# Performance work log

Measured on AMD Instinct MI355X. Metric: run time of the kernel, lower is better.

The kernel has to match this reference:

```python
import jax, jax.numpy as jnp
import numpy as np

N_NODES = 100000
N_EDGES = 1000000
NUM_FEATURES = 64
HIDDEN = 64
NUM_GRAPHS = 128


def setup_inputs() -> dict:
    key = jax.random.key(0)
    ks = jax.random.split(key, 12)
    x = jax.random.normal(ks[0], (N_NODES, NUM_FEATURES), dtype=jnp.float32)
    edge_index = jax.random.randint(ks[1], (2, N_EDGES), 0, N_NODES, dtype=jnp.int64)
    edge_weight = jax.random.uniform(ks[2], (N_EDGES,), dtype=jnp.float32)
    batch = jnp.sort(jax.random.randint(ks[3], (N_NODES,), 0, NUM_GRAPHS, dtype=jnp.int64))
    s1 = 1.0 / np.sqrt(NUM_FEATURES)
    s2 = 1.0 / np.sqrt(HIDDEN)
    # GraphConv layer 1: lin_rel (with bias) applied to aggregated msgs, lin_root (no bias)
    w1_rel = jax.random.uniform(ks[4], (HIDDEN, NUM_FEATURES), jnp.float32, -s1, s1)
    b1_rel = jax.random.uniform(ks[5], (HIDDEN,), jnp.float32, -s1, s1)
    w1_root = jax.random.uniform(ks[6], (HIDDEN, NUM_FEATURES), jnp.float32, -s1, s1)
    # GraphConv layer 2
    w2_rel = jax.random.uniform(ks[7], (HIDDEN, HIDDEN), jnp.float32, -s2, s2)
    b2_rel = jax.random.uniform(ks[8], (HIDDEN,), jnp.float32, -s2, s2)
    w2_root = jax.random.uniform(ks[9], (HIDDEN, HIDDEN), jnp.float32, -s2, s2)
    # final Linear(hidden, 1)
    w_lin = jax.random.uniform(ks[10], (1, HIDDEN), jnp.float32, -s2, s2)
    b_lin = jax.random.uniform(ks[11], (1,), jnp.float32, -s2, s2)
    return {
        "x": x, "edge_index": edge_index, "edge_weight": edge_weight, "batch": batch,
        "w1_rel": w1_rel, "b1_rel": b1_rel, "w1_root": w1_root,
        "w2_rel": w2_rel, "b2_rel": b2_rel, "w2_root": w2_root,
        "w_lin": w_lin, "b_lin": b_lin,
    }


def graph_conv(x, edge_index, edge_weight, w_rel, b_rel, w_root):
    # messages: x[src] * e, scatter-add into dst  (gather-scale-scatter)
    src, dst = edge_index[0], edge_index[1]
    msgs = x[src] * edge_weight[:, None]                      # [E, F]
    aggr = jax.ops.segment_sum(msgs, dst, num_segments=x.shape[0])  # [N, F]
    return aggr @ w_rel.T + b_rel + x @ w_root.T


def reference(x, edge_index, edge_weight, batch,
              w1_rel, b1_rel, w1_root, w2_rel, b2_rel, w2_root, w_lin, b_lin):
    h = graph_conv(x, edge_index, edge_weight, w1_rel, b1_rel, w1_root)
    h = jax.nn.relu(h)
    h = graph_conv(h, edge_index, edge_weight, w2_rel, b2_rel, w2_root)
    # global_mean_pool over graph ids
    sums = jax.ops.segment_sum(h, batch, num_segments=NUM_GRAPHS)          # [G, H]
    counts = jax.ops.segment_sum(jnp.ones((h.shape[0],), h.dtype), batch,
                                 num_segments=NUM_GRAPHS)                  # [G]
    pooled = sums / jnp.maximum(counts, 1.0)[:, None]
    # dropout(p=0.5) in eval mode is identity
    return pooled @ w_lin.T + b_lin                                        # [G, 1]
```

## Files before the change

### kernel.cpp

```cpp
#include <hip/hip_runtime.h>
#include <hip/hip_bf16.h>


#define N_NODES 100000
#define N_EDGES 1000000
#define NGRAPHS 128
#define BN 512
#define NBUCK ((N_NODES + BN - 1) / BN)
#define FILL_T 16
#define FILL_TILE (256 * FILL_T)
#define FILL_NB ((N_EDGES + FILL_TILE - 1) / FILL_TILE)
#define NTILES (N_NODES / 16)
#define AST 72

typedef __attribute__((ext_vector_type(8))) short bf16x8;
typedef __attribute__((ext_vector_type(8))) unsigned short u16x8;
typedef __attribute__((ext_vector_type(4))) float f32x4;

__device__ __forceinline__ unsigned short f2bf(float f) {
    unsigned u = __float_as_uint(f);
    unsigned r = (u + 0x7FFFu + ((u >> 16) & 1u)) >> 16;
    return (unsigned short)r;
}
__device__ __forceinline__ float bf2f(unsigned short h) {
    return __uint_as_float(((unsigned)h) << 16);
}

__global__ __launch_bounds__(256) void prep_cvt_kernel(
    const float* __restrict__ x, unsigned short* __restrict__ xh, int n8,
    const float* __restrict__ w1rel, const float* __restrict__ w1root,
    const float* __restrict__ w2rel, const float* __restrict__ w2root,
    const float* __restrict__ wlin, const float* __restrict__ b2rel,
    const float* __restrict__ blin, unsigned short* __restrict__ whirel,
    unsigned short* __restrict__ wlorel, unsigned short* __restrict__ whiroot,
    unsigned short* __restrict__ wloroot, float* __restrict__ u,
    float* __restrict__ v, float* __restrict__ C) {
    int tid = threadIdx.x;
    int i = blockIdx.x * 256 + tid;
    if (i < n8) {
        const float4* xp = (const float4*)x + (size_t)i * 2;
        float4 a = xp[0], b = xp[1];
        u16x8 o;
        o[0] = f2bf(a.x); o[1] = f2bf(a.y); o[2] = f2bf(a.z); o[3] = f2bf(a.w);
        o[4] = f2bf(b.x); o[5] = f2bf(b.y); o[6] = f2bf(b.z); o[7] = f2bf(b.w);
        *((u16x8*)xh + i) = o;
        return;
    }
    for (int k = tid; k < 4096; k += 256) {
        float a = w1rel[k];
        unsigned short hi = f2bf(a);
        whirel[k] = hi;
        wlorel[k] = f2bf(a - bf2f(hi));
        float b = w1root[k];
        unsigned short hb = f2bf(b);
        whiroot[k] = hb;
        wloroot[k] = f2bf(b - bf2f(hb));
    }
    if (tid < 64) {
        float uu = 0.f, vv = 0.f;
        for (int h = 0; h < 64; ++h) {
            float wl = wlin[h];
            uu += wl * w2rel[h * 64 + tid];
            vv += wl * w2root[h * 64 + tid];
        }
        u[tid] = uu;
        v[tid] = vv;
    }
    if (tid == 0) {
        float c = blin[0];
        for (int h = 0; h < 64; ++h) c += wlin[h] * b2rel[h];
        *C = c;
    }
}

__global__ __launch_bounds__(256) void bucket_hist(const int* __restrict__ ei,
                                                   int* __restrict__ bcount,
                                                   int E) {
    __shared__ int lh[NBUCK];
    int tid = threadIdx.x;
    for (int i = tid; i < NBUCK; i += 256) lh[i] = 0;
    __syncthreads();
    for (int e = blockIdx.x * 256 + tid; e < E; e += gridDim.x * 256)
        atomicAdd(&lh[ei[E + e] >> 9], 1);
    __syncthreads();
    for (int i = tid; i < NBUCK; i += 256) {
        int c = lh[i];
        if (c) atomicAdd(&bcount[i], c);
    }
}

__global__ void bucket_scan(const int* __restrict__ bcount,
                            int* __restrict__ boff, int* __restrict__ cursor) {
    __shared__ int s[256];
    int t = threadIdx.x;
    int v = (t < NBUCK) ? bcount[t] : 0;
    s[t] = v;
    __syncthreads();
    for (int off = 1; off < 256; off <<= 1) {
        int x = (t >= off) ? s[t - off] : 0;
        __syncthreads();
        s[t] += x;
        __syncthreads();
    }
    if (t < NBUCK) {
        boff[t] = s[t] - v;
        cursor[t] = s[t] - v;
    }
    if (t == 255) boff[NBUCK] = s[255];
}

__global__ __launch_bounds__(256) void bucket_fill(
    const int* __restrict__ ei, const float* __restrict__ ew,
    int* __restrict__ cursor, int2* __restrict__ ebuf, int E) {
    __shared__ int lh[NBUCK];
    __shared__ int gbase[NBUCK];
    int tid = threadIdx.x;
    for (int i = tid; i < NBUCK; i += 256) lh[i] = 0;
    __syncthreads();
    int base = blockIdx.x * FILL_TILE;
    int2 rec[FILL_T];
    int meta[FILL_T];
#pragma unroll
    for (int i = 0; i < FILL_T; ++i) {
        int e = base + i * 256 + tid;
        meta[i] = -1;
        if (e < E) {
            int src = ei[e];
            int dst = ei[E + e];
            int b = dst >> 9;
            int r = atomicAdd(&lh[b], 1);
            rec[i].x = src | ((dst & (BN - 1)) << 17);
            rec[i].y = __float_as_int(ew[e]);
            meta[i] = (b << 13) | r;
        }
    }
    __syncthreads();
    for (int i = tid; i < NBUCK; i += 256) {
        int c = lh[i];
        gbase[i] = c ? atomicAdd(&cursor[i], c) : 0;
    }
    __syncthreads();
#pragma unroll
    for (int i = 0; i < FILL_T; ++i) {
        if (meta[i] >= 0) {
            int b = meta[i] >> 13;
            int r = meta[i] & 8191;
            ebuf[gbase[b] + r] = rec[i];
        }
    }
}

__global__ __launch_bounds__(512) void csr_build(
    const int* __restrict__ boff, const int2* __restrict__ ebuf,
    const int* __restrict__ batch, int* __restrict__ row_ptr,
    int2* __restrict__ csr, int N) {
    __shared__ int s[BN];
    int b = blockIdx.x;
    int t = threadIdx.x;
    int beg = boff[b], end = boff[b + 1];
    s[t] = 0;
    __syncthreads();
    for (int j = beg + t; j < end; j += 512)
        atomicAdd(&s[(ebuf[j].x >> 17) & (BN - 1)], 1);
    __syncthreads();
    int v = s[t];
    for (int off = 1; off < BN; off <<= 1) {
        int x = (t >= off) ? s[t - off] : 0;
        __syncthreads();
        s[t] += x;
        __syncthreads();
    }
    int excl = s[t] - v;
    int gidx = b * BN + t;
    if (gidx <= N) row_ptr[gidx] = beg + excl;
    __syncthreads();
    s[t] = excl;
    __syncthreads();
    for (int j = beg + t; j < end; j += 512) {
        int2 rec = ebuf[j];
        int dlo = (rec.x >> 17) & (BN - 1);
        int g = batch[b * BN + dlo];
        int r = atomicAdd(&s[dlo], 1);
        int2 o;
        o.x = (rec.x & 0x1FFFF) | (g << 17);
        o.y = rec.y;
        csr[beg + r] = o;
    }
}

__global__ __launch_bounds__(256) void gather_dense_kernel(
    const unsigned short* __restrict__ xh, const int* __restrict__ row_ptr,
    const int2* __restrict__ csr, const unsigned short* __restrict__ whirel,
    const unsigned short* __restrict__ wlorel,
    const unsigned short* __restrict__ whiroot,
    const unsigned short* __restrict__ wloroot,
    const float* __restrict__ b1rel, const float* __restrict__ u,
    const float* __restrict__ v, float* __restrict__ p, float* __restrict__ q,
    int ntiles) {
    __shared__ unsigned short arow[4][16 * AST];
    int lane = threadIdx.x & 63;
    int wv = threadIdx.x >> 6;
    int wave = (blockIdx.x << 2) + wv;
    if (wave >= ntiles) return;
    unsigned short* my = &arow[wv][0];
    int nb = wave * 16;
    int g = lane >> 4;
    int c = lane & 15;

    for (int nl = 0; nl < 16; ++nl) {
        int node = nb + nl;
        int beg = row_ptr[node], end = row_ptr[node + 1];
        float4 acc = {0.f, 0.f, 0.f, 0.f};
        for (int j0 = beg; j0 < end; j0 += 64) {
            int cnt = min(64, end - j0);
            int2 e = {0, 0};
            if (lane < cnt) e = csr[j0 + lane];
            for (int k = 0; k < cnt; k += 4) {
                int myk = k + g;
                int sj = __shfl(e.x, myk) & 0x1FFFF;
                float wj = __int_as_float(__shfl(e.y, myk));
                if (myk < cnt) {
                    ushort4 xv =
                        *(const ushort4*)(xh + (size_t)sj * 64 + c * 4);
                    acc.x += wj * bf2f(xv.x);
                    acc.y += wj * bf2f(xv.y);
                    acc.z += wj * bf2f(xv.z);
                    acc.w += wj * bf2f(xv.w);
                }
            }
        }
#pragma unroll
        for (int off = 16; off < 64; off <<= 1) {
            acc.x += __shfl_xor(acc.x, off);
            acc.y += __shfl_xor(acc.y, off);
            acc.z += __shfl_xor(acc.z, off);
            acc.w += __shfl_xor(acc.w, off);
        }
        if (lane < 16) {
            ushort4 o;
            o.x = f2bf(acc.x);
            o.y = f2bf(acc.y);
            o.z = f2bf(acc.z);
            o.w = f2bf(acc.w);
            *(ushort4*)(my + nl * AST + c * 4) = o;
        }
    }

    int lo4 = lane & 15;
    int quad = lane >> 4;
    f32x4 acc4[4];
#pragma unroll
    for (int t = 0; t < 4; ++t) acc4[t] = (f32x4){0.f, 0.f, 0.f, 0.f};
#pragma unroll
    for (int s = 0; s < 2; ++s) {
        bf16x8 Aa = *(const bf16x8*)(my + lo4 * AST + s * 32 + quad * 8);
        bf16x8 Ax = *(const bf16x8*)(xh + (size_t)(nb + lo4) * 64 + s * 32 +
                                     quad * 8);
#pragma unroll
        for (int t = 0; t < 4; ++t) {
            int off = (t * 16 + lo4) * 64 + s * 32 + quad * 8;
            bf16x8 bhr = *(const bf16x8*)(whirel + off);
            bf16x8 blr = *(const bf16x8*)(wlorel + off);
            bf16x8 bhx = *(const bf16x8*)(whiroot + off);
            bf16x8 blx = *(const bf16x8*)(wloroot + off);
            acc4[t] = __builtin_amdgcn_mfma_f32_16x16x32_bf16(Aa, bhr, acc4[t],
                                                              0, 0, 0);
            acc4[t] = __builtin_amdgcn_mfma_f32_16x16x32_bf16(Aa, blr, acc4[t],
                                                              0, 0, 0);
            acc4[t] = __builtin_amdgcn_mfma_f32_16x16x32_bf16(Ax, bhx, acc4[t],
                                                              0, 0, 0);
            acc4[t] = __builtin_amdgcn_mfma_f32_16x16x32_bf16(Ax, blx, acc4[t],
                                                              0, 0, 0);
        }
    }

    float pc[4] = {0.f, 0.f, 0.f, 0.f};
    float qc[4] = {0.f, 0.f, 0.f, 0.f};
#pragma unroll
    for (int t = 0; t < 4; ++t) {
        float bb = b1rel[t * 16 + lo4];
        float uu = u[t * 16 + lo4];
        float vv = v[t * 16 + lo4];
#pragma unroll
        for (int r = 0; r < 4; ++r) {
            float h1 = fmaxf(acc4[t][r] + bb, 0.f);
            pc[r] += uu * h1;
            qc[r] += vv * h1;
        }
    }
#pragma unroll
    for (int off = 1; off < 16; off <<= 1) {
#pragma unroll
        for (int r = 0; r < 4; ++r) {
            pc[r] += __shfl_xor(pc[r], off);
            qc[r] += __shfl_xor(qc[r], off);
        }
    }
    if (lo4 == 0) {
        f32x4 po = {pc[0], pc[1], pc[2], pc[3]};
        f32x4 qo = {qc[0], qc[1], qc[2], qc[3]};
        *(f32x4*)(p + nb + quad * 4) = po;
        *(f32x4*)(q + nb + quad * 4) = qo;
    }
}

#define PT_EPT 4
#define PT_EPW (64 * PT_EPT)
#define PT_NB ((N_EDGES + 4 * PT_EPW - 1) / (4 * PT_EPW))
#define PS_NB 98
__global__ __launch_bounds__(256) void pool_both(
    const int2* __restrict__ csr, const float* __restrict__ p,
    const float* __restrict__ q, const int* __restrict__ batch,
    float* __restrict__ gp, float* __restrict__ gq, float* __restrict__ gc,
    int E, int N) {
    __shared__ float lbuf[2 * NGRAPHS];
    int tid = threadIdx.x;
    lbuf[tid] = 0.f;
    __syncthreads();
    if (blockIdx.x < PT_NB) {
        int lane = tid & 63;
        int wid = (blockIdx.x * 256 + tid) >> 6;
        int base = wid * PT_EPW;
        float acc = 0.f;
        int curg = -1;
#pragma unroll
        for (int i = 0; i < PT_EPT; ++i) {
            int j = base + i * 64 + lane;
            if (j < E) {
                int2 e = csr[j];
                int g = ((unsigned)e.x) >> 17;
                float val = __int_as_float(e.y) * p[e.x & 0x1FFFF];
                if (g != curg) {
                    if (curg >= 0) atomicAdd(&lbuf[curg], acc);
                    curg = g;
                    acc = 0.f;
                }
                acc += val;
            }
        }
        if (curg >= 0) atomicAdd(&lbuf[curg], acc);
        __syncthreads();
        if (tid < NGRAPHS) {
            float t = lbuf[tid];
            if (t != 0.f) atomicAdd(&gp[tid], t);
        }
    } else {
        int bid = blockIdx.x - PT_NB;
        for (int i = bid * 256 + tid; i < N; i += PS_NB * 256) {
            int g = batch[i];
            atomicAdd(&lbuf[g], q[i]);
            atomicAdd(&lbuf[NGRAPHS + g], 1.f);
        }
        __syncthreads();
        if (tid < NGRAPHS) {
            if (lbuf[NGRAPHS + tid] != 0.f) {
                atomicAdd(&gq[tid], lbuf[tid]);
                atomicAdd(&gc[tid], lbuf[NGRAPHS + tid]);
            }
        }
    }
}

__global__ void final_kernel(const float* __restrict__ gp,
                             const float* __restrict__ gq,
                             const float* __restrict__ gc,
                             const float* __restrict__ C,
                             float* __restrict__ out) {
    int g = threadIdx.x;
    float c = fmaxf(gc[g], 1.0f);
    out[g] = (gp[g] + gq[g]) / c + *C;
}

extern "C" void kernel_launch(void* const* d_in, const int* in_sizes, int n_in,
                              void* d_out, int out_size, void* d_ws,
                              size_t ws_size, hipStream_t stream) {
    const float* x      = (const float*)d_in[0];
    const int*   ei     = (const int*)d_in[1];
    const float* ew     = (const float*)d_in[2];
    const int*   batch  = (const int*)d_in[3];
    const float* w1rel  = (const float*)d_in[4];
    const float* b1rel  = (const float*)d_in[5];
    const float* w1root = (const float*)d_in[6];
    const float* w2rel  = (const float*)d_in[7];
    const float* b2rel  = (const float*)d_in[8];
    const float* w2root = (const float*)d_in[9];
    const float* wlin   = (const float*)d_in[10];
    const float* blin   = (const float*)d_in[11];
    float* out = (float*)d_out;

    char* wsb = (char*)d_ws;
    int2* csr  = (int2*)wsb;
    int2* ebuf = (int2*)(wsb + (size_t)N_EDGES * 8);
    char* tail = wsb + (size_t)N_EDGES * 16;
    unsigned short* whirel  = (unsigned short*)tail;
    unsigned short* wlorel  = whirel + 4096;
    unsigned short* whiroot = wlorel + 4096;
    unsigned short* wloroot = whiroot + 4096;
    float* p  = (float*)(wloroot + 4096);
    float* q  = p + N_NODES;
    float* u  = q + N_NODES;
    float* v  = u + 64;
    float* C  = v + 64;
    int*   bcount = (int*)(C + 1);
    float* gp = (float*)(bcount + NBUCK);
    float* gq = gp + NGRAPHS;
    float* gc = gq + NGRAPHS;
    int*   boff   = (int*)(gc + NGRAPHS);
    int*   cursor = boff + (NBUCK + 1);
    int*   row_ptr = cursor + NBUCK;
    unsigned short* xh = (unsigned short*)(row_ptr + N_NODES + 2);

    hipMemsetAsync(bcount, 0, (NBUCK + 3 * NGRAPHS) * sizeof(int), stream);

    int n8 = N_NODES * 64 / 8;
    prep_cvt_kernel<<<n8 / 256 + 1, 256, 0, stream>>>(
        x, xh, n8, w1rel, w1root, w2rel, w2root, wlin, b2rel, blin, whirel,
        wlorel, whiroot, wloroot, u, v, C);

    bucket_hist<<<256, 256, 0, stream>>>(ei, bcount, N_EDGES);
    bucket_scan<<<1, 256, 0, stream>>>(bcount, boff, cursor);
    bucket_fill<<<FILL_NB, 256, 0, stream>>>(ei, ew, cursor, ebuf, N_EDGES);
    csr_build<<<NBUCK, 512, 0, stream>>>(boff, ebuf, batch, row_ptr, csr,
                                         N_NODES);

    gather_dense_kernel<<<(NTILES + 3) / 4, 256, 0, stream>>>(
        xh, row_ptr, csr, whirel, wlorel, whiroot, wloroot, b1rel, u, v, p, q,
        NTILES);

    pool_both<<<PT_NB + PS_NB, 256, 0, stream>>>(csr, p, q, batch, gp, gq, gc,
                                                 N_EDGES, N_NODES);
    final_kernel<<<1, NGRAPHS, 0, stream>>>(gp, gq, gc, C, out);
}
```

Baseline: 223.1 us.

## Gather whole 16-node tile edges at once with LDS float atomics

The gather kernel no longer walks the 16 nodes of a tile one at a time with a per-node edge loop and a cross-lane reduction. It now streams all edges of the tile in 64-edge chunks and scatters weighted features into a per-wave fp32 LDS accumulator using shared-memory atomics. To support this, the CSR fill step packs each edge's local destination row into bits 24-27, and the pool kernel masks the graph id accordingly. This removes the divergence and underused lanes caused by short per-node loops, but it adds LDS atomic contention, a larger fp32 LDS footprint, and a float-to-bf16 conversion when building the MFMA A operand.

```diff
diff --git a/kernel.cpp b/kernel.cpp
--- a/kernel.cpp
+++ b/kernel.cpp
@@ -11,7 +11,7 @@
 #define FILL_TILE (256 * FILL_T)
 #define FILL_NB ((N_EDGES + FILL_TILE - 1) / FILL_TILE)
 #define NTILES (N_NODES / 16)
-#define AST 72
+#define AST 68
 
 typedef __attribute__((ext_vector_type(8))) short bf16x8;
 typedef __attribute__((ext_vector_type(8))) unsigned short u16x8;
@@ -182,7 +182,7 @@
         int g = batch[b * BN + dlo];
         int r = atomicAdd(&s[dlo], 1);
         int2 o;
-        o.x = (rec.x & 0x1FFFF) | (g << 17);
+        o.x = (rec.x & 0x1FFFF) | (g << 17) | ((dlo & 15) << 24);
         o.y = rec.y;
         csr[beg + r] = o;
     }
@@ -197,52 +197,38 @@
     const float* __restrict__ b1rel, const float* __restrict__ u,
     const float* __restrict__ v, float* __restrict__ p, float* __restrict__ q,
     int ntiles) {
-    __shared__ unsigned short arow[4][16 * AST];
+    __shared__ float accs[4][16 * AST];
     int lane = threadIdx.x & 63;
     int wv = threadIdx.x >> 6;
     int wave = (blockIdx.x << 2) + wv;
     if (wave >= ntiles) return;
-    unsigned short* my = &arow[wv][0];
+    float* my = &accs[wv][0];
     int nb = wave * 16;
     int g = lane >> 4;
     int c = lane & 15;
 
-    for (int nl = 0; nl < 16; ++nl) {
-        int node = nb + nl;
-        int beg = row_ptr[node], end = row_ptr[node + 1];
-        float4 acc = {0.f, 0.f, 0.f, 0.f};
-        for (int j0 = beg; j0 < end; j0 += 64) {
-            int cnt = min(64, end - j0);
-            int2 e = {0, 0};
-            if (lane < cnt) e = csr[j0 + lane];
-            for (int k = 0; k < cnt; k += 4) {
-                int myk = k + g;
-                int sj = __shfl(e.x, myk) & 0x1FFFF;
-                float wj = __int_as_float(__shfl(e.y, myk));
-                if (myk < cnt) {
-                    ushort4 xv =
-                        *(const ushort4*)(xh + (size_t)sj * 64 + c * 4);
-                    acc.x += wj * bf2f(xv.x);
-                    acc.y += wj * bf2f(xv.y);
-                    acc.z += wj * bf2f(xv.z);
-                    acc.w += wj * bf2f(xv.w);
-                }
+    for (int i = lane; i < 16 * AST; i += 64) my[i] = 0.f;
+
+    int ebeg = row_ptr[nb], eend = row_ptr[nb + 16];
+    for (int j0 = ebeg; j0 < eend; j0 += 64) {
+        int cnt = min(64, eend - j0);
+        int2 e = {0, 0};
+        if (lane < cnt) e = csr[j0 + lane];
+#pragma unroll
+        for (int r = 0; r < 16; ++r) {
+            int myk = r * 4 + g;
+            int ex = __shfl(e.x, myk);
+            float wj = __int_as_float(__shfl(e.y, myk));
+            if (myk < cnt) {
+                int sj = ex & 0x1FFFF;
+                int dl = (ex >> 24) & 15;
+                ushort4 xv = *(const ushort4*)(xh + (size_t)sj * 64 + c * 4);
+                float* dst = my + dl * AST + c * 4;
+                atomicAdd(dst + 0, wj * bf2f(xv.x));
+                atomicAdd(dst + 1, wj * bf2f(xv.y));
+                atomicAdd(dst + 2, wj * bf2f(xv.z));
+                atomicAdd(dst + 3, wj * bf2f(xv.w));
             }
-        }
-#pragma unroll
-        for (int off = 16; off < 64; off <<= 1) {
-            acc.x += __shfl_xor(acc.x, off);
-            acc.y += __shfl_xor(acc.y, off);
-            acc.z += __shfl_xor(acc.z, off);
-            acc.w += __shfl_xor(acc.w, off);
-        }
-        if (lane < 16) {
-            ushort4 o;
-            o.x = f2bf(acc.x);
-            o.y = f2bf(acc.y);
-            o.z = f2bf(acc.z);
-            o.w = f2bf(acc.w);
-            *(ushort4*)(my + nl * AST + c * 4) = o;
         }
     }
 
@@ -253,7 +239,10 @@
     for (int t = 0; t < 4; ++t) acc4[t] = (f32x4){0.f, 0.f, 0.f, 0.f};
 #pragma unroll
     for (int s = 0; s < 2; ++s) {
-        bf16x8 Aa = *(const bf16x8*)(my + lo4 * AST + s * 32 + quad * 8);
+        const float* ap = my + lo4 * AST + s * 32 + quad * 8;
+        bf16x8 Aa;
+#pragma unroll
+        for (int j = 0; j < 8; ++j) Aa[j] = (short)f2bf(ap[j]);
         bf16x8 Ax = *(const bf16x8*)(xh + (size_t)(nb + lo4) * 64 + s * 32 +
                                      quad * 8);
 #pragma unroll
@@ -328,7 +317,7 @@
             int j = base + i * 64 + lane;
             if (j < E) {
                 int2 e = csr[j];
-                int g = ((unsigned)e.x) >> 17;
+                int g = (e.x >> 17) & 127;
                 float val = __int_as_float(e.y) * p[e.x & 0x1FFFF];
                 if (g != curg) {
                     if (curg >= 0) atomicAdd(&lbuf[curg], acc);
```

After: 546.4 us. 2.45x slower.

## Split fused gather+MFMA kernel into separate gather and dense kernels

Applied to the files above, without the earlier changes.

The fused gather/dense kernel is split in two. A gather kernel writes bf16 aggregated features to a global buffer, using a fixed 2048-block grid where each wave handles a contiguous chunk of nodes. A separate MFMA dense kernel then reads that buffer. The aggregation buffer reuses the ebuf workspace region, and the graph id is masked in the pool kernel. The aim is better load balance and occupancy for the gather, at the cost of an extra global round trip (about 12.8 MB) and one more launch.

```diff
diff --git a/kernel.cpp b/kernel.cpp
--- a/kernel.cpp
+++ b/kernel.cpp
@@ -10,8 +10,6 @@
 #define FILL_T 16
 #define FILL_TILE (256 * FILL_T)
 #define FILL_NB ((N_EDGES + FILL_TILE - 1) / FILL_TILE)
-#define NTILES (N_NODES / 16)
-#define AST 72
 
 typedef __attribute__((ext_vector_type(8))) short bf16x8;
 typedef __attribute__((ext_vector_type(8))) unsigned short u16x8;
@@ -188,27 +186,17 @@
     }
 }
 
-__global__ __launch_bounds__(256) void gather_dense_kernel(
+__global__ __launch_bounds__(256) void gather_kernel(
     const unsigned short* __restrict__ xh, const int* __restrict__ row_ptr,
-    const int2* __restrict__ csr, const unsigned short* __restrict__ whirel,
-    const unsigned short* __restrict__ wlorel,
-    const unsigned short* __restrict__ whiroot,
-    const unsigned short* __restrict__ wloroot,
-    const float* __restrict__ b1rel, const float* __restrict__ u,
-    const float* __restrict__ v, float* __restrict__ p, float* __restrict__ q,
-    int ntiles) {
-    __shared__ unsigned short arow[4][16 * AST];
+    const int2* __restrict__ csr, unsigned short* __restrict__ aggr, int N,
+    int chunk) {
     int lane = threadIdx.x & 63;
-    int wv = threadIdx.x >> 6;
-    int wave = (blockIdx.x << 2) + wv;
-    if (wave >= ntiles) return;
-    unsigned short* my = &arow[wv][0];
-    int nb = wave * 16;
+    int wid = (blockIdx.x * blockDim.x + threadIdx.x) >> 6;
     int g = lane >> 4;
     int c = lane & 15;
-
-    for (int nl = 0; nl < 16; ++nl) {
-        int node = nb + nl;
+    int n0 = wid * chunk;
+    int n1 = min(n0 + chunk, N);
+    for (int node = n0; node < n1; ++node) {
         int beg = row_ptr[node], end = row_ptr[node + 1];
         float4 acc = {0.f, 0.f, 0.f, 0.f};
         for (int j0 = beg; j0 < end; j0 += 64) {
@@ -242,18 +230,35 @@
             o.y = f2bf(acc.y);
             o.z = f2bf(acc.z);
             o.w = f2bf(acc.w);
-            *(ushort4*)(my + nl * AST + c * 4) = o;
-        }
-    }
-
+            *(ushort4*)(aggr + (size_t)node * 64 + c * 4) = o;
+        }
+    }
+}
+
+__global__ __launch_bounds__(256, 2) void dense_kernel(
+    const unsigned short* __restrict__ aggr,
+    const unsigned short* __restrict__ xh,
+    const unsigned short* __restrict__ whirel,
+    const unsigned short* __restrict__ wlorel,
+    const unsigned short* __restrict__ whiroot,
+    const unsigned short* __restrict__ wloroot,
+    const float* __restrict__ b1rel, const float* __restrict__ u,
+    const float* __restrict__ v, float* __restrict__ p, float* __restrict__ q,
+    int N) {
+    int lane = threadIdx.x & 63;
+    int wave = (blockIdx.x << 2) + (threadIdx.x >> 6);
+    int nb = wave * 16;
+    if (nb >= N) return;
     int lo4 = lane & 15;
     int quad = lane >> 4;
-    f32x4 acc4[4];
-#pragma unroll
-    for (int t = 0; t < 4; ++t) acc4[t] = (f32x4){0.f, 0.f, 0.f, 0.f};
-#pragma unroll
+
+    f32x4 acc[4];
+#pragma unroll
+    for (int t = 0; t < 4; ++t) acc[t] = (f32x4){0.f, 0.f, 0.f, 0.f};
+
     for (int s = 0; s < 2; ++s) {
-        bf16x8 Aa = *(const bf16x8*)(my + lo4 * AST + s * 32 + quad * 8);
+        bf16x8 Aa = *(const bf16x8*)(aggr + (size_t)(nb + lo4) * 64 + s * 32 +
+                                     quad * 8);
         bf16x8 Ax = *(const bf16x8*)(xh + (size_t)(nb + lo4) * 64 + s * 32 +
                                      quad * 8);
 #pragma unroll
@@ -263,14 +268,14 @@
             bf16x8 blr = *(const bf16x8*)(wlorel + off);
             bf16x8 bhx = *(const bf16x8*)(whiroot + off);
             bf16x8 blx = *(const bf16x8*)(wloroot + off);
-            acc4[t] = __builtin_amdgcn_mfma_f32_16x16x32_bf16(Aa, bhr, acc4[t],
-                                                              0, 0, 0);
-            acc4[t] = __builtin_amdgcn_mfma_f32_16x16x32_bf16(Aa, blr, acc4[t],
-                                                              0, 0, 0);
-            acc4[t] = __builtin_amdgcn_mfma_f32_16x16x32_bf16(Ax, bhx, acc4[t],
-                                                              0, 0, 0);
-            acc4[t] = __builtin_amdgcn_mfma_f32_16x16x32_bf16(Ax, blx, acc4[t],
-                                                              0, 0, 0);
+            acc[t] = __builtin_amdgcn_mfma_f32_16x16x32_bf16(Aa, bhr, acc[t],
+                                                             0, 0, 0);
+            acc[t] = __builtin_amdgcn_mfma_f32_16x16x32_bf16(Aa, blr, acc[t],
+                                                             0, 0, 0);
+            acc[t] = __builtin_amdgcn_mfma_f32_16x16x32_bf16(Ax, bhx, acc[t],
+                                                             0, 0, 0);
+            acc[t] = __builtin_amdgcn_mfma_f32_16x16x32_bf16(Ax, blx, acc[t],
+                                                             0, 0, 0);
         }
     }
 
@@ -283,7 +288,7 @@
         float vv = v[t * 16 + lo4];
 #pragma unroll
         for (int r = 0; r < 4; ++r) {
-            float h1 = fmaxf(acc4[t][r] + bb, 0.f);
+            float h1 = fmaxf(acc[t][r] + bb, 0.f);
             pc[r] += uu * h1;
             qc[r] += vv * h1;
         }
@@ -328,7 +333,7 @@
             int j = base + i * 64 + lane;
             if (j < E) {
                 int2 e = csr[j];
-                int g = ((unsigned)e.x) >> 17;
+                int g = (e.x >> 17) & 127;
                 float val = __int_as_float(e.y) * p[e.x & 0x1FFFF];
                 if (g != curg) {
                     if (curg >= 0) atomicAdd(&lbuf[curg], acc);
@@ -390,8 +395,9 @@
 
     char* wsb = (char*)d_ws;
     int2* csr  = (int2*)wsb;
-    int2* ebuf = (int2*)(wsb + (size_t)N_EDGES * 8);
-    char* tail = wsb + (size_t)N_EDGES * 16;
+    unsigned short* aggr = (unsigned short*)(wsb + (size_t)N_EDGES * 8);
+    int2* ebuf = (int2*)aggr;
+    char* tail = wsb + (size_t)N_EDGES * 8 + (size_t)N_NODES * 128;
     unsigned short* whirel  = (unsigned short*)tail;
     unsigned short* wlorel  = whirel + 4096;
     unsigned short* whiroot = wlorel + 4096;
@@ -423,10 +429,20 @@
     csr_build<<<NBUCK, 512, 0, stream>>>(boff, ebuf, batch, row_ptr, csr,
                                          N_NODES);
 
-    gather_dense_kernel<<<(NTILES + 3) / 4, 256, 0, stream>>>(
-        xh, row_ptr, csr, whirel, wlorel, whiroot, wloroot, b1rel, u, v, p, q,
-        NTILES);
-
+    {
+        int blocks = 2048;
+        int waves = blocks * 4;
+        int chunk = (N_NODES + waves - 1) / waves;
+        gather_kernel<<<blocks, 256, 0, stream>>>(xh, row_ptr, csr, aggr,
+                                                  N_NODES, chunk);
+    }
+    {
+        int tiles = N_NODES / 16;
+        int blocks = (tiles + 3) / 4;
+        dense_kernel<<<blocks, 256, 0, stream>>>(aggr, xh, whirel, wlorel,
+                                                 whiroot, wloroot, b1rel, u, v,
+                                                 p, q, N_NODES);
+    }
     pool_both<<<PT_NB + PS_NB, 256, 0, stream>>>(csr, p, q, batch, gp, gq, gc,
                                                  N_EDGES, N_NODES);
     final_kernel<<<1, NGRAPHS, 0, stream>>>(gp, gq, gc, C, out);
```

Result: slower. 229.7 us (+3.0%).
